# Performance work log

Hardware: AMD Instinct MI355X
Metric: run time of the kernel (lower is better)

The kernel has to match this reference:

```python
import jax, jax.numpy as jnp
import numpy as np

ODIM = 8192      # output dim (slice target)
MSIZE = 64       # tile size
N_BLOCKS = 1024  # size of shared block bank


def setup_inputs() -> dict:
    key = jax.random.key(0)
    k1, k2, k3, k4 = jax.random.split(key, 4)
    x = jax.random.normal(k1, (256, 8192), dtype=jnp.float32)
    # bank of msize x msize module blocks (scaled like fan-in init)
    blocks = jax.random.normal(k2, (N_BLOCKS, MSIZE, MSIZE), dtype=jnp.float32) * 0.02
    bound = 1.0 / np.sqrt(ODIM).astype(np.float32)
    bias = jax.random.uniform(k3, (ODIM,), dtype=jnp.float32, minval=-bound, maxval=bound)
    # parts: [icount, ocount] indices into the block bank
    parts = jax.random.randint(k4, (128, 128), 0, N_BLOCKS)
    return {"x": x, "blocks": blocks, "bias": bias, "parts": parts}


def reference(x, blocks, bias, parts):
    icount, ocount = parts.shape
    m = blocks.shape[-1]
    # build_mosaic: gather blocks per parts and tile into a dense weight matrix
    fc = blocks[parts]                                   # [ic, oc, m, m]
    fc_mat = fc.transpose(0, 2, 1, 3).reshape(icount * m, ocount * m)
    # idim (8192) is divisible by msize, so pad is identity (rem == 0 branch)
    y = x @ fc_mat                                       # [B, oc*m]
    y = y[..., :ODIM] + bias                             # slice + bias; post = Identity
    return y
```

## Files before the change

kernel.cpp:

```cpp
#include <hip/hip_runtime.h>
#include <stdint.h>

#define BATCH 256
#define IDIM  8192
#define ODIM  8192
#define MS    64
#define IC    128
#define OC    128
#define NB    1024

#define TM 128
#define TN 128
#define KSPLIT 4
#define IB_PER (IC / KSPLIT)

typedef __bf16 bf16x8 __attribute__((ext_vector_type(8)));
typedef float  floatx4 __attribute__((ext_vector_type(4)));

__device__ __forceinline__ void async_load16(unsigned short* lds_p, const unsigned short* g_p) {
    __builtin_amdgcn_global_load_lds(
        (const __attribute__((address_space(1))) unsigned int*)g_p,
        (__attribute__((address_space(3))) unsigned int*)lds_p,
        16, 0, 0);
}

__device__ __forceinline__ unsigned short f32_to_bf16(float f) {
    unsigned int u = __float_as_uint(f);
    u += 0x7FFFu + ((u >> 16) & 1u);
    return (unsigned short)(u >> 16);
}

__global__ void k_convert(const float* __restrict__ x, const float* __restrict__ blocks,
                          unsigned short* __restrict__ xb, unsigned short* __restrict__ bt) {
    __shared__ float tile[MS][MS + 1];
    int b = blockIdx.x;
    if (b < NB) {
        const float4* src4 = (const float4*)(blocks + (size_t)b * MS * MS);
        unsigned short* dst = bt + (size_t)b * MS * MS;
        #pragma unroll
        for (int i = 0; i < 4; ++i) {
            int slot = i * 256 + threadIdx.x;
            int r = slot >> 4, c4 = (slot & 15) * 4;
            float4 v = src4[slot];
            tile[r][c4 + 0] = v.x; tile[r][c4 + 1] = v.y;
            tile[r][c4 + 2] = v.z; tile[r][c4 + 3] = v.w;
        }
        __syncthreads();
        #pragma unroll
        for (int i = 0; i < 2; ++i) {
            int slot = i * 256 + threadIdx.x;
            int c = slot >> 3, o = slot & 7;
            union { unsigned short s[8]; uint4 v; } u;
            #pragma unroll
            for (int j = 0; j < 8; ++j) u.s[j] = f32_to_bf16(tile[o * 8 + j][c]);
            *(uint4*)(dst + c * MS + o * 8) = u.v;
        }
    } else {
        int t = (b - NB) * 256 + threadIdx.x;
        const float4* x4 = (const float4*)x;
        float4 a = x4[2 * t], bb = x4[2 * t + 1];
        union { unsigned short s[8]; uint4 v; } u;
        u.s[0] = f32_to_bf16(a.x);  u.s[1] = f32_to_bf16(a.y);
        u.s[2] = f32_to_bf16(a.z);  u.s[3] = f32_to_bf16(a.w);
        u.s[4] = f32_to_bf16(bb.x); u.s[5] = f32_to_bf16(bb.y);
        u.s[6] = f32_to_bf16(bb.z); u.s[7] = f32_to_bf16(bb.w);
        ((uint4*)xb)[t] = u.v;
    }
}

__global__ __launch_bounds__(256, 2)
void k_mosaic_gemm(const unsigned short* __restrict__ xb,
                   const unsigned short* __restrict__ bt,
                   const int* __restrict__ parts,
                   float* __restrict__ partial) {
    __shared__ __align__(16) unsigned short a_lds[TM * MS];
    __shared__ __align__(16) unsigned short b_lds[TN * MS];

    const int tid  = threadIdx.x;
    const int lane = tid & 63;
    const int wave = tid >> 6;
    const int wrow = wave >> 1;
    const int wcol = wave & 1;
    const int nt = blockIdx.x;
    const int mt = blockIdx.y;
    const int ks = blockIdx.z;

    const int m0  = mt * TM;
    const int ob0 = nt * (TN / MS);
    const int ib0 = ks * IB_PER;

    const int row  = lane & 15;
    const int quad = lane >> 4;

    int a_off[2][4], b_off[2][4];
    #pragma unroll
    for (int kk = 0; kk < 2; ++kk) {
        int oct = kk * 4 + quad;
        #pragma unroll
        for (int mi = 0; mi < 4; ++mi) {
            int r = wrow * 64 + mi * 16 + row;
            a_off[kk][mi] = r * MS + ((oct ^ (r & 7)) << 3);
        }
        #pragma unroll
        for (int ni = 0; ni < 4; ++ni) {
            int n = wcol * 64 + ni * 16 + row;
            b_off[kk][ni] = n * MS + ((oct ^ (n & 7)) << 3);
        }
    }

    floatx4 acc[4][4];
    #pragma unroll
    for (int mi = 0; mi < 4; ++mi)
        #pragma unroll
        for (int ni = 0; ni < 4; ++ni)
            acc[mi][ni] = (floatx4){0.f, 0.f, 0.f, 0.f};

    for (int ib = ib0; ib < ib0 + IB_PER; ++ib) {
        int p0 = parts[ib * OC + ob0];
        int p1 = parts[ib * OC + ob0 + 1];

        #pragma unroll
        for (int j = 0; j < 4; ++j) {
            int slot = j * 256 + tid;
            int m = slot >> 3;
            int oct = (slot & 7) ^ (m & 7);
            async_load16(&a_lds[slot * 8],
                         xb + (size_t)(m0 + m) * IDIM + ib * MS + oct * 8);
        }
        #pragma unroll
        for (int j = 0; j < 4; ++j) {
            int slot = j * 256 + tid;
            int n = slot >> 3;
            int oct = (slot & 7) ^ (n & 7);
            int p = (j < 2) ? p0 : p1;
            async_load16(&b_lds[slot * 8],
                         bt + (size_t)p * (MS * MS) + (n & 63) * MS + oct * 8);
        }
        __syncthreads();

        #pragma unroll
        for (int kk = 0; kk < 2; ++kk) {
            bf16x8 af[4], bfr[4];
            #pragma unroll
            for (int mi = 0; mi < 4; ++mi)
                af[mi] = *(const bf16x8*)&a_lds[a_off[kk][mi]];
            #pragma unroll
            for (int ni = 0; ni < 4; ++ni)
                bfr[ni] = *(const bf16x8*)&b_lds[b_off[kk][ni]];
            #pragma unroll
            for (int mi = 0; mi < 4; ++mi)
                #pragma unroll
                for (int ni = 0; ni < 4; ++ni)
                    acc[mi][ni] = __builtin_amdgcn_mfma_f32_16x16x32_bf16(
                        af[mi], bfr[ni], acc[mi][ni], 0, 0, 0);
        }
        __syncthreads();
    }

    float* out = partial + (size_t)ks * BATCH * ODIM;
    #pragma unroll
    for (int mi = 0; mi < 4; ++mi)
        #pragma unroll
        for (int ni = 0; ni < 4; ++ni)
            #pragma unroll
            for (int r = 0; r < 4; ++r) {
                int rowg = m0 + wrow * 64 + mi * 16 + quad * 4 + r;
                int colg = nt * TN + wcol * 64 + ni * 16 + row;
                out[(size_t)rowg * ODIM + colg] = acc[mi][ni][r];
            }
}

__global__ void k_reduce_bias(const float* __restrict__ partial,
                              const float* __restrict__ bias,
                              float* __restrict__ out) {
    int t = blockIdx.x * 256 + threadIdx.x;
    const float4* b4 = (const float4*)bias;
    float4 c = b4[t & (ODIM / 4 - 1)];
    float4 r = {c.x, c.y, c.z, c.w};
    #pragma unroll
    for (int k = 0; k < KSPLIT; ++k) {
        const float4* p = (const float4*)(partial + (size_t)k * BATCH * ODIM);
        float4 a = p[t];
        r.x += a.x; r.y += a.y; r.z += a.z; r.w += a.w;
    }
    ((float4*)out)[t] = r;
}

extern "C" void kernel_launch(void* const* d_in, const int* in_sizes, int n_in,
                              void* d_out, int out_size, void* d_ws, size_t ws_size,
                              hipStream_t stream) {
    const float* x      = (const float*)d_in[0];
    const float* blocks = (const float*)d_in[1];
    const float* bias   = (const float*)d_in[2];
    const int*   parts  = (const int*)d_in[3];
    float* out = (float*)d_out;

    char* ws = (char*)d_ws;
    unsigned short* xb      = (unsigned short*)ws;
    unsigned short* btb     = (unsigned short*)(ws + (4u << 20));
    float*          partial = (float*)(ws + (12u << 20));

    k_convert<<<NB + (BATCH * IDIM) / (256 * 8), 256, 0, stream>>>(x, blocks, xb, btb);
    k_mosaic_gemm<<<dim3(ODIM / TN, BATCH / TM, KSPLIT), 256, 0, stream>>>(xb, btb, parts, partial);
    k_reduce_bias<<<(BATCH * ODIM) / (256 * 4), 256, 0, stream>>>(partial, bias, out);
}
```

Measured before the change: 125.5 us.

## Replace split-K partial buffer and reduce kernel with atomic accumulation into output

Removes the separate reduce+bias kernel and the partial-sum workspace. The output is initialised with bias inside the convert kernel, and the GEMM accumulates split-K results into it with float atomicAdd. The M tile grows to the full batch (256) and KSPLIT doubles to 8, which keeps the block count the same and lets each block reuse its B tile across all rows. The cost is atomic traffic, nondeterministic summation order, and roughly double the accumulator registers per thread, which may reduce occupancy.

```diff
diff --git a/kernel.cpp b/kernel.cpp
--- a/kernel.cpp
+++ b/kernel.cpp
@@ -9,9 +9,9 @@
 #define OC    128
 #define NB    1024
 
-#define TM 128
+#define TM 256
 #define TN 128
-#define KSPLIT 4
+#define KSPLIT 8
 #define IB_PER (IC / KSPLIT)
 
 typedef __bf16 bf16x8 __attribute__((ext_vector_type(8)));
@@ -30,8 +30,11 @@
     return (unsigned short)(u >> 16);
 }
 
+#define XCONV_BLKS ((BATCH * IDIM) / (256 * 8))
 __global__ void k_convert(const float* __restrict__ x, const float* __restrict__ blocks,
-                          unsigned short* __restrict__ xb, unsigned short* __restrict__ bt) {
+                          const float* __restrict__ bias,
+                          unsigned short* __restrict__ xb, unsigned short* __restrict__ bt,
+                          float* __restrict__ out) {
     __shared__ float tile[MS][MS + 1];
     int b = blockIdx.x;
     if (b < NB) {
@@ -55,7 +58,7 @@
             for (int j = 0; j < 8; ++j) u.s[j] = f32_to_bf16(tile[o * 8 + j][c]);
             *(uint4*)(dst + c * MS + o * 8) = u.v;
         }
-    } else {
+    } else if (b < NB + XCONV_BLKS) {
         int t = (b - NB) * 256 + threadIdx.x;
         const float4* x4 = (const float4*)x;
         float4 a = x4[2 * t], bb = x4[2 * t + 1];
@@ -65,6 +68,15 @@
         u.s[4] = f32_to_bf16(bb.x); u.s[5] = f32_to_bf16(bb.y);
         u.s[6] = f32_to_bf16(bb.z); u.s[7] = f32_to_bf16(bb.w);
         ((uint4*)xb)[t] = u.v;
+    } else {
+        int r = b - NB - XCONV_BLKS;
+        const float4* b4 = (const float4*)bias;
+        float4* o4 = (float4*)out + (size_t)r * (ODIM / 4);
+        #pragma unroll
+        for (int j = 0; j < 8; ++j) {
+            int c = j * 256 + threadIdx.x;
+            o4[c] = b4[c];
+        }
     }
 }
 
@@ -72,7 +84,7 @@
 void k_mosaic_gemm(const unsigned short* __restrict__ xb,
                    const unsigned short* __restrict__ bt,
                    const int* __restrict__ parts,
-                   float* __restrict__ partial) {
+                   float* __restrict__ out) {
     __shared__ __align__(16) unsigned short a_lds[TM * MS];
     __shared__ __align__(16) unsigned short b_lds[TN * MS];
 
@@ -82,23 +94,21 @@
     const int wrow = wave >> 1;
     const int wcol = wave & 1;
     const int nt = blockIdx.x;
-    const int mt = blockIdx.y;
-    const int ks = blockIdx.z;
+    const int ks = blockIdx.y;
 
-    const int m0  = mt * TM;
     const int ob0 = nt * (TN / MS);
     const int ib0 = ks * IB_PER;
 
     const int row  = lane & 15;
     const int quad = lane >> 4;
 
-    int a_off[2][4], b_off[2][4];
+    int a_off[2][8], b_off[2][4];
     #pragma unroll
     for (int kk = 0; kk < 2; ++kk) {
         int oct = kk * 4 + quad;
         #pragma unroll
-        for (int mi = 0; mi < 4; ++mi) {
-            int r = wrow * 64 + mi * 16 + row;
+        for (int mi = 0; mi < 8; ++mi) {
+            int r = wrow * 128 + mi * 16 + row;
             a_off[kk][mi] = r * MS + ((oct ^ (r & 7)) << 3);
         }
         #pragma unroll
@@ -108,9 +118,9 @@
         }
     }
 
-    floatx4 acc[4][4];
+    floatx4 acc[8][4];
     #pragma unroll
-    for (int mi = 0; mi < 4; ++mi)
+    for (int mi = 0; mi < 8; ++mi)
         #pragma unroll
         for (int ni = 0; ni < 4; ++ni)
             acc[mi][ni] = (floatx4){0.f, 0.f, 0.f, 0.f};
@@ -120,12 +130,12 @@
         int p1 = parts[ib * OC + ob0 + 1];
 
         #pragma unroll
-        for (int j = 0; j < 4; ++j) {
+        for (int j = 0; j < 8; ++j) {
             int slot = j * 256 + tid;
             int m = slot >> 3;
             int oct = (slot & 7) ^ (m & 7);
             async_load16(&a_lds[slot * 8],
-                         xb + (size_t)(m0 + m) * IDIM + ib * MS + oct * 8);
+                         xb + (size_t)m * IDIM + ib * MS + oct * 8);
         }
         #pragma unroll
         for (int j = 0; j < 4; ++j) {
@@ -140,15 +150,15 @@
 
         #pragma unroll
         for (int kk = 0; kk < 2; ++kk) {
-            bf16x8 af[4], bfr[4];
+            bf16x8 af[8], bfr[4];
             #pragma unroll
-            for (int mi = 0; mi < 4; ++mi)
+            for (int mi = 0; mi < 8; ++mi)
                 af[mi] = *(const bf16x8*)&a_lds[a_off[kk][mi]];
             #pragma unroll
             for (int ni = 0; ni < 4; ++ni)
                 bfr[ni] = *(const bf16x8*)&b_lds[b_off[kk][ni]];
             #pragma unroll
-            for (int mi = 0; mi < 4; ++mi)
+            for (int mi = 0; mi < 8; ++mi)
                 #pragma unroll
                 for (int ni = 0; ni < 4; ++ni)
                     acc[mi][ni] = __builtin_amdgcn_mfma_f32_16x16x32_bf16(
@@ -157,33 +167,16 @@
         __syncthreads();
     }
 
-    float* out = partial + (size_t)ks * BATCH * ODIM;
     #pragma unroll
-    for (int mi = 0; mi < 4; ++mi)
+    for (int mi = 0; mi < 8; ++mi)
         #pragma unroll
         for (int ni = 0; ni < 4; ++ni)
             #pragma unroll
             for (int r = 0; r < 4; ++r) {
-                int rowg = m0 + wrow * 64 + mi * 16 + quad * 4 + r;
+                int rowg = wrow * 128 + mi * 16 + quad * 4 + r;
                 int colg = nt * TN + wcol * 64 + ni * 16 + row;
-                out[(size_t)rowg * ODIM + colg] = acc[mi][ni][r];
+                atomicAdd(&out[(size_t)rowg * ODIM + colg], acc[mi][ni][r]);
             }
-}
-
-__global__ void k_reduce_bias(const float* __restrict__ partial,
-                              const float* __restrict__ bias,
-                              float* __restrict__ out) {
-    int t = blockIdx.x * 256 + threadIdx.x;
-    const float4* b4 = (const float4*)bias;
-    float4 c = b4[t & (ODIM / 4 - 1)];
-    float4 r = {c.x, c.y, c.z, c.w};
-    #pragma unroll
-    for (int k = 0; k < KSPLIT; ++k) {
-        const float4* p = (const float4*)(partial + (size_t)k * BATCH * ODIM);
-        float4 a = p[t];
-        r.x += a.x; r.y += a.y; r.z += a.z; r.w += a.w;
-    }
-    ((float4*)out)[t] = r;
 }
 
 extern "C" void kernel_launch(void* const* d_in, const int* in_sizes, int n_in,
@@ -196,11 +189,9 @@
     float* out = (float*)d_out;
 
     char* ws = (char*)d_ws;
-    unsigned short* xb      = (unsigned short*)ws;
-    unsigned short* btb     = (unsigned short*)(ws + (4u << 20));
-    float*          partial = (float*)(ws + (12u << 20));
+    unsigned short* xb  = (unsigned short*)ws;
+    unsigned short* btb = (unsigned short*)(ws + (4u << 20));
 
-    k_convert<<<NB + (BATCH * IDIM) / (256 * 8), 256, 0, stream>>>(x, blocks, xb, btb);
-    k_mosaic_gemm<<<dim3(ODIM / TN, BATCH / TM, KSPLIT), 256, 0, stream>>>(xb, btb, parts, partial);
-    k_reduce_bias<<<(BATCH * ODIM) / (256 * 4), 256, 0, stream>>>(partial, bias, out);
+    k_convert<<<NB + XCONV_BLKS + BATCH, 256, 0, stream>>>(x, blocks, bias, xb, btb, out);
+    k_mosaic_gemm<<<dim3(ODIM / TN, KSPLIT), 256, 0, stream>>>(xb, btb, parts, out);
 }
```

Result: slower. 153.7 us (+22.5%).

## Pre-swizzle operands into MFMA fragment layout and load directly to registers

Applied to the files above, without the earlier changes.

The convert kernel now writes x and the block bank in MFMA fragment order and transposes the parts table, so the GEMM can drop LDS staging and barriers and load bf16x8 fragments straight from global memory into registers. The GEMM becomes a per-64-column tile over all 256 rows (4 waves, each 64 rows), with register double-buffering of the next two K blocks. This removes the LDS round trip and syncthreads, but A is no longer shared through LDS across waves. Each workgroup reads the full A slice from global/L2, and the grid shrinks to 512 workgroups.

```diff
diff --git a/kernel.cpp b/kernel.cpp
--- a/kernel.cpp
+++ b/kernel.cpp
@@ -9,20 +9,11 @@
 #define OC    128
 #define NB    1024
 
-#define TM 128
-#define TN 128
 #define KSPLIT 4
-#define IB_PER (IC / KSPLIT)
+#define NIB (IC / KSPLIT)
 
 typedef __bf16 bf16x8 __attribute__((ext_vector_type(8)));
 typedef float  floatx4 __attribute__((ext_vector_type(4)));
-
-__device__ __forceinline__ void async_load16(unsigned short* lds_p, const unsigned short* g_p) {
-    __builtin_amdgcn_global_load_lds(
-        (const __attribute__((address_space(1))) unsigned int*)g_p,
-        (__attribute__((address_space(3))) unsigned int*)lds_p,
-        16, 0, 0);
-}
 
 __device__ __forceinline__ unsigned short f32_to_bf16(float f) {
     unsigned int u = __float_as_uint(f);
@@ -30,13 +21,16 @@
     return (unsigned short)(u >> 16);
 }
 
+#define XCONV_BLKS 1024
+#define PT_BLKS 64
 __global__ void k_convert(const float* __restrict__ x, const float* __restrict__ blocks,
-                          unsigned short* __restrict__ xb, unsigned short* __restrict__ bt) {
+                          const int* __restrict__ parts,
+                          unsigned short* __restrict__ xa, unsigned short* __restrict__ bbuf,
+                          int* __restrict__ pT) {
     __shared__ float tile[MS][MS + 1];
     int b = blockIdx.x;
     if (b < NB) {
         const float4* src4 = (const float4*)(blocks + (size_t)b * MS * MS);
-        unsigned short* dst = bt + (size_t)b * MS * MS;
         #pragma unroll
         for (int i = 0; i < 4; ++i) {
             int slot = i * 256 + threadIdx.x;
@@ -46,67 +40,63 @@
             tile[r][c4 + 2] = v.z; tile[r][c4 + 3] = v.w;
         }
         __syncthreads();
+        unsigned short* dst = bbuf + (size_t)b * 4096;
         #pragma unroll
         for (int i = 0; i < 2; ++i) {
-            int slot = i * 256 + threadIdx.x;
-            int c = slot >> 3, o = slot & 7;
+            int oo = i * 256 + threadIdx.x;
+            int L = oo & 63, kk = (oo >> 6) & 1, ng = (oo >> 7) & 3;
+            int row = L & 15, quad = L >> 4;
             union { unsigned short s[8]; uint4 v; } u;
             #pragma unroll
-            for (int j = 0; j < 8; ++j) u.s[j] = f32_to_bf16(tile[o * 8 + j][c]);
-            *(uint4*)(dst + c * MS + o * 8) = u.v;
+            for (int j = 0; j < 8; ++j)
+                u.s[j] = f32_to_bf16(tile[kk * 32 + quad * 8 + j][ng * 16 + row]);
+            *(uint4*)(dst + oo * 8) = u.v;
         }
+    } else if (b < NB + XCONV_BLKS) {
+        int o = (b - NB) * 256 + threadIdx.x;
+        int L = o & 63, kk = (o >> 6) & 1, ib = (o >> 7) & 127, g = o >> 14;
+        int m  = g * 16 + (L & 15);
+        int k0 = ib * 64 + kk * 32 + (L >> 4) * 8;
+        const float* src = x + (size_t)m * IDIM + k0;
+        float4 a = *(const float4*)src, c = *(const float4*)(src + 4);
+        union { unsigned short s[8]; uint4 v; } u;
+        u.s[0] = f32_to_bf16(a.x); u.s[1] = f32_to_bf16(a.y);
+        u.s[2] = f32_to_bf16(a.z); u.s[3] = f32_to_bf16(a.w);
+        u.s[4] = f32_to_bf16(c.x); u.s[5] = f32_to_bf16(c.y);
+        u.s[6] = f32_to_bf16(c.z); u.s[7] = f32_to_bf16(c.w);
+        *(uint4*)(xa + (size_t)o * 8) = u.v;
     } else {
-        int t = (b - NB) * 256 + threadIdx.x;
-        const float4* x4 = (const float4*)x;
-        float4 a = x4[2 * t], bb = x4[2 * t + 1];
-        union { unsigned short s[8]; uint4 v; } u;
-        u.s[0] = f32_to_bf16(a.x);  u.s[1] = f32_to_bf16(a.y);
-        u.s[2] = f32_to_bf16(a.z);  u.s[3] = f32_to_bf16(a.w);
-        u.s[4] = f32_to_bf16(bb.x); u.s[5] = f32_to_bf16(bb.y);
-        u.s[6] = f32_to_bf16(bb.z); u.s[7] = f32_to_bf16(bb.w);
-        ((uint4*)xb)[t] = u.v;
+        int t = (b - NB - XCONV_BLKS) * 256 + threadIdx.x;
+        int oc = t >> 7, ic = t & 127;
+        pT[t] = parts[ic * OC + oc];
     }
 }
 
 __global__ __launch_bounds__(256, 2)
-void k_mosaic_gemm(const unsigned short* __restrict__ xb,
-                   const unsigned short* __restrict__ bt,
-                   const int* __restrict__ parts,
+void k_mosaic_gemm(const unsigned short* __restrict__ xa,
+                   const unsigned short* __restrict__ bbuf,
+                   const int* __restrict__ pT,
                    float* __restrict__ partial) {
-    __shared__ __align__(16) unsigned short a_lds[TM * MS];
-    __shared__ __align__(16) unsigned short b_lds[TN * MS];
-
     const int tid  = threadIdx.x;
     const int lane = tid & 63;
-    const int wave = tid >> 6;
-    const int wrow = wave >> 1;
-    const int wcol = wave & 1;
-    const int nt = blockIdx.x;
-    const int mt = blockIdx.y;
-    const int ks = blockIdx.z;
-
-    const int m0  = mt * TM;
-    const int ob0 = nt * (TN / MS);
-    const int ib0 = ks * IB_PER;
+    const int w    = tid >> 6;
+    const int ob   = blockIdx.x;
+    const int ks   = blockIdx.y;
+    const int ib0  = ks * NIB;
 
     const int row  = lane & 15;
     const int quad = lane >> 4;
 
-    int a_off[2][4], b_off[2][4];
+    const unsigned short* abase[4][2];
     #pragma unroll
-    for (int kk = 0; kk < 2; ++kk) {
-        int oct = kk * 4 + quad;
+    for (int mi = 0; mi < 4; ++mi)
         #pragma unroll
-        for (int mi = 0; mi < 4; ++mi) {
-            int r = wrow * 64 + mi * 16 + row;
-            a_off[kk][mi] = r * MS + ((oct ^ (r & 7)) << 3);
-        }
-        #pragma unroll
-        for (int ni = 0; ni < 4; ++ni) {
-            int n = wcol * 64 + ni * 16 + row;
-            b_off[kk][ni] = n * MS + ((oct ^ (n & 7)) << 3);
-        }
-    }
+        for (int kk = 0; kk < 2; ++kk)
+            abase[mi][kk] = xa + (size_t)(w * 4 + mi) * 131072 + kk * 512 + lane * 8;
+
+    const int* pp = pT + ob * 128 + ib0;
+
+    bf16x8 ac[4][2], bc[4][2], an[4][2], bn[4][2];
 
     floatx4 acc[4][4];
     #pragma unroll
@@ -115,46 +105,33 @@
         for (int ni = 0; ni < 4; ++ni)
             acc[mi][ni] = (floatx4){0.f, 0.f, 0.f, 0.f};
 
-    for (int ib = ib0; ib < ib0 + IB_PER; ++ib) {
-        int p0 = parts[ib * OC + ob0];
-        int p1 = parts[ib * OC + ob0 + 1];
+#define LOAD_A(dst, ib_) do { \
+    _Pragma("unroll") for (int mi = 0; mi < 4; ++mi) \
+    _Pragma("unroll") for (int kk = 0; kk < 2; ++kk) \
+        dst[mi][kk] = *(const bf16x8*)(abase[mi][kk] + (size_t)(ib0 + (ib_)) * 1024); } while (0)
+#define LOAD_B(dst, p_) do { \
+    const unsigned short* bp = bbuf + (size_t)(p_) * 4096 + lane * 8; \
+    _Pragma("unroll") for (int ng = 0; ng < 4; ++ng) \
+    _Pragma("unroll") for (int kk = 0; kk < 2; ++kk) \
+        dst[ng][kk] = *(const bf16x8*)(bp + (ng * 2 + kk) * 512); } while (0)
+#define DO_MFMA(a_, b_) do { \
+    _Pragma("unroll") for (int kk = 0; kk < 2; ++kk) \
+    _Pragma("unroll") for (int mi = 0; mi < 4; ++mi) \
+    _Pragma("unroll") for (int ni = 0; ni < 4; ++ni) \
+        acc[mi][ni] = __builtin_amdgcn_mfma_f32_16x16x32_bf16(a_[mi][kk], b_[ni][kk], acc[mi][ni], 0, 0, 0); } while (0)
 
-        #pragma unroll
-        for (int j = 0; j < 4; ++j) {
-            int slot = j * 256 + tid;
-            int m = slot >> 3;
-            int oct = (slot & 7) ^ (m & 7);
-            async_load16(&a_lds[slot * 8],
-                         xb + (size_t)(m0 + m) * IDIM + ib * MS + oct * 8);
-        }
-        #pragma unroll
-        for (int j = 0; j < 4; ++j) {
-            int slot = j * 256 + tid;
-            int n = slot >> 3;
-            int oct = (slot & 7) ^ (n & 7);
-            int p = (j < 2) ? p0 : p1;
-            async_load16(&b_lds[slot * 8],
-                         bt + (size_t)p * (MS * MS) + (n & 63) * MS + oct * 8);
-        }
-        __syncthreads();
+    LOAD_A(ac, 0);
+    LOAD_B(bc, pp[0]);
 
-        #pragma unroll
-        for (int kk = 0; kk < 2; ++kk) {
-            bf16x8 af[4], bfr[4];
-            #pragma unroll
-            for (int mi = 0; mi < 4; ++mi)
-                af[mi] = *(const bf16x8*)&a_lds[a_off[kk][mi]];
-            #pragma unroll
-            for (int ni = 0; ni < 4; ++ni)
-                bfr[ni] = *(const bf16x8*)&b_lds[b_off[kk][ni]];
-            #pragma unroll
-            for (int mi = 0; mi < 4; ++mi)
-                #pragma unroll
-                for (int ni = 0; ni < 4; ++ni)
-                    acc[mi][ni] = __builtin_amdgcn_mfma_f32_16x16x32_bf16(
-                        af[mi], bfr[ni], acc[mi][ni], 0, 0, 0);
-        }
-        __syncthreads();
+    for (int ii = 0; ii < NIB; ii += 2) {
+        int i1 = (ii + 1 < NIB) ? ii + 1 : NIB - 1;
+        int i2 = (ii + 2 < NIB) ? ii + 2 : NIB - 1;
+        LOAD_A(an, i1);
+        LOAD_B(bn, pp[i1]);
+        DO_MFMA(ac, bc);
+        LOAD_A(ac, i2);
+        LOAD_B(bc, pp[i2]);
+        DO_MFMA(an, bn);
     }
 
     float* out = partial + (size_t)ks * BATCH * ODIM;
@@ -164,8 +141,8 @@
         for (int ni = 0; ni < 4; ++ni)
             #pragma unroll
             for (int r = 0; r < 4; ++r) {
-                int rowg = m0 + wrow * 64 + mi * 16 + quad * 4 + r;
-                int colg = nt * TN + wcol * 64 + ni * 16 + row;
+                int rowg = w * 64 + mi * 16 + quad * 4 + r;
+                int colg = ob * 64 + ni * 16 + row;
                 out[(size_t)rowg * ODIM + colg] = acc[mi][ni][r];
             }
 }
@@ -196,11 +173,12 @@
     float* out = (float*)d_out;
 
     char* ws = (char*)d_ws;
-    unsigned short* xb      = (unsigned short*)ws;
-    unsigned short* btb     = (unsigned short*)(ws + (4u << 20));
-    float*          partial = (float*)(ws + (12u << 20));
+    unsigned short* xa      = (unsigned short*)ws;
+    unsigned short* bbuf    = (unsigned short*)(ws + (4u << 20));
+    int*            pTr     = (int*)(ws + (12u << 20));
+    float*          partial = (float*)(ws + (13u << 20));
 
-    k_convert<<<NB + (BATCH * IDIM) / (256 * 8), 256, 0, stream>>>(x, blocks, xb, btb);
-    k_mosaic_gemm<<<dim3(ODIM / TN, BATCH / TM, KSPLIT), 256, 0, stream>>>(xb, btb, parts, partial);
+    k_convert<<<NB + XCONV_BLKS + PT_BLKS, 256, 0, stream>>>(x, blocks, parts, xa, bbuf, pTr);
+    k_mosaic_gemm<<<dim3(OC, KSPLIT), 256, 0, stream>>>(xa, bbuf, pTr, partial);
     k_reduce_bias<<<(BATCH * ODIM) / (256 * 4), 256, 0, stream>>>(partial, bias, out);
 }
```

Result: slower. 153.2 us (+22.1%).

## Double-buffer LDS tiles and prefetch transposed parts indices via shuffles

Applied to the files above, without the earlier changes.

Converts the GEMM main loop to a two-stage LDS double buffer: the next K-block's async global-to-LDS loads are issued before computing the current one, using a partial vmcnt wait instead of a full sync. The parts index table is transposed in the convert kernel so each wave loads all its block indices up front and broadcasts them with shuffles, removing per-iteration scalar index loads. This doubles LDS use per workgroup, which may limit occupancy under the 2-block launch bound.

```diff
diff --git a/kernel.cpp b/kernel.cpp
--- a/kernel.cpp
+++ b/kernel.cpp
@@ -12,10 +12,12 @@
 #define TM 128
 #define TN 128
 #define KSPLIT 4
-#define IB_PER (IC / KSPLIT)
+#define NIB (IC / KSPLIT)
 
 typedef __bf16 bf16x8 __attribute__((ext_vector_type(8)));
 typedef float  floatx4 __attribute__((ext_vector_type(4)));
+
+#define WAITCNT_VM(n) ((((n) & 15) | (((n) >> 4) << 14)) | 0x70 | 0xF00)
 
 __device__ __forceinline__ void async_load16(unsigned short* lds_p, const unsigned short* g_p) {
     __builtin_amdgcn_global_load_lds(
@@ -30,8 +32,12 @@
     return (unsigned short)(u >> 16);
 }
 
+#define XCONV_BLKS 1024
+#define PT_BLKS 64
 __global__ void k_convert(const float* __restrict__ x, const float* __restrict__ blocks,
-                          unsigned short* __restrict__ xb, unsigned short* __restrict__ bt) {
+                          const int* __restrict__ parts,
+                          unsigned short* __restrict__ xb, unsigned short* __restrict__ bt,
+                          int* __restrict__ pT) {
     __shared__ float tile[MS][MS + 1];
     int b = blockIdx.x;
     if (b < NB) {
@@ -55,7 +61,7 @@
             for (int j = 0; j < 8; ++j) u.s[j] = f32_to_bf16(tile[o * 8 + j][c]);
             *(uint4*)(dst + c * MS + o * 8) = u.v;
         }
-    } else {
+    } else if (b < NB + XCONV_BLKS) {
         int t = (b - NB) * 256 + threadIdx.x;
         const float4* x4 = (const float4*)x;
         float4 a = x4[2 * t], bb = x4[2 * t + 1];
@@ -65,16 +71,20 @@
         u.s[4] = f32_to_bf16(bb.x); u.s[5] = f32_to_bf16(bb.y);
         u.s[6] = f32_to_bf16(bb.z); u.s[7] = f32_to_bf16(bb.w);
         ((uint4*)xb)[t] = u.v;
+    } else {
+        int t = (b - NB - XCONV_BLKS) * 256 + threadIdx.x;
+        int oc = t >> 7, ic = t & 127;
+        pT[t] = parts[ic * OC + oc];
     }
 }
 
 __global__ __launch_bounds__(256, 2)
 void k_mosaic_gemm(const unsigned short* __restrict__ xb,
                    const unsigned short* __restrict__ bt,
-                   const int* __restrict__ parts,
+                   const int* __restrict__ pT,
                    float* __restrict__ partial) {
-    __shared__ __align__(16) unsigned short a_lds[TM * MS];
-    __shared__ __align__(16) unsigned short b_lds[TN * MS];
+    __shared__ __align__(16) unsigned short a_lds[2][TM * MS];
+    __shared__ __align__(16) unsigned short b_lds[2][TN * MS];
 
     const int tid  = threadIdx.x;
     const int lane = tid & 63;
@@ -86,11 +96,18 @@
     const int ks = blockIdx.z;
 
     const int m0  = mt * TM;
-    const int ob0 = nt * (TN / MS);
-    const int ib0 = ks * IB_PER;
+    const int ob0 = nt * 2;
+    const int ib0 = ks * NIB;
 
     const int row  = lane & 15;
     const int quad = lane >> 4;
+
+    int pv0 = 0, pv1 = 0;
+    {
+        int li = lane & 31;
+        pv0 = pT[ob0 * IC + ib0 + li];
+        pv1 = pT[(ob0 + 1) * IC + ib0 + li];
+    }
 
     int a_off[2][4], b_off[2][4];
     #pragma unroll
@@ -115,47 +132,59 @@
         for (int ni = 0; ni < 4; ++ni)
             acc[mi][ni] = (floatx4){0.f, 0.f, 0.f, 0.f};
 
-    for (int ib = ib0; ib < ib0 + IB_PER; ++ib) {
-        int p0 = parts[ib * OC + ob0];
-        int p1 = parts[ib * OC + ob0 + 1];
-
-        #pragma unroll
-        for (int j = 0; j < 4; ++j) {
-            int slot = j * 256 + tid;
-            int m = slot >> 3;
-            int oct = (slot & 7) ^ (m & 7);
-            async_load16(&a_lds[slot * 8],
-                         xb + (size_t)(m0 + m) * IDIM + ib * MS + oct * 8);
-        }
-        #pragma unroll
-        for (int j = 0; j < 4; ++j) {
-            int slot = j * 256 + tid;
-            int n = slot >> 3;
-            int oct = (slot & 7) ^ (n & 7);
-            int p = (j < 2) ? p0 : p1;
-            async_load16(&b_lds[slot * 8],
-                         bt + (size_t)p * (MS * MS) + (n & 63) * MS + oct * 8);
-        }
-        __syncthreads();
-
-        #pragma unroll
-        for (int kk = 0; kk < 2; ++kk) {
-            bf16x8 af[4], bfr[4];
-            #pragma unroll
-            for (int mi = 0; mi < 4; ++mi)
-                af[mi] = *(const bf16x8*)&a_lds[a_off[kk][mi]];
-            #pragma unroll
-            for (int ni = 0; ni < 4; ++ni)
-                bfr[ni] = *(const bf16x8*)&b_lds[b_off[kk][ni]];
-            #pragma unroll
-            for (int mi = 0; mi < 4; ++mi)
-                #pragma unroll
-                for (int ni = 0; ni < 4; ++ni)
-                    acc[mi][ni] = __builtin_amdgcn_mfma_f32_16x16x32_bf16(
-                        af[mi], bfr[ni], acc[mi][ni], 0, 0, 0);
-        }
-        __syncthreads();
-    }
+#define STAGE(buf, ib_, p0_, p1_) do {                                        \
+    _Pragma("unroll")                                                         \
+    for (int j = 0; j < 4; ++j) {                                             \
+        int slot = j * 256 + tid;                                             \
+        int m = slot >> 3;                                                    \
+        int oct = (slot & 7) ^ (m & 7);                                       \
+        async_load16(&a_lds[buf][slot * 8],                                   \
+                     xb + (size_t)(m0 + m) * IDIM + (ib_) * MS + oct * 8);    \
+    }                                                                         \
+    _Pragma("unroll")                                                         \
+    for (int j = 0; j < 4; ++j) {                                             \
+        int slot = j * 256 + tid;                                             \
+        int n = slot >> 3;                                                    \
+        int oct = (slot & 7) ^ (n & 7);                                       \
+        int p = (j < 2) ? (p0_) : (p1_);                                      \
+        async_load16(&b_lds[buf][slot * 8],                                   \
+                     bt + (size_t)p * (MS * MS) + (n & 63) * MS + oct * 8);   \
+    } } while (0)
+
+#define COMPUTE(buf) do {                                                     \
+    _Pragma("unroll")                                                         \
+    for (int kk = 0; kk < 2; ++kk) {                                          \
+        bf16x8 af[4], bfr[4];                                                 \
+        _Pragma("unroll")                                                     \
+        for (int mi = 0; mi < 4; ++mi)                                        \
+            af[mi] = *(const bf16x8*)&a_lds[buf][a_off[kk][mi]];              \
+        _Pragma("unroll")                                                     \
+        for (int ni = 0; ni < 4; ++ni)                                        \
+            bfr[ni] = *(const bf16x8*)&b_lds[buf][b_off[kk][ni]];             \
+        _Pragma("unroll")                                                     \
+        for (int mi = 0; mi < 4; ++mi)                                        \
+            _Pragma("unroll")                                                 \
+            for (int ni = 0; ni < 4; ++ni)                                    \
+                acc[mi][ni] = __builtin_amdgcn_mfma_f32_16x16x32_bf16(        \
+                    af[mi], bfr[ni], acc[mi][ni], 0, 0, 0);                   \
+    } } while (0)
+
+    {
+        int p0 = __shfl(pv0, 0), p1 = __shfl(pv1, 0);
+        STAGE(0, ib0 + 0, p0, p1);
+    }
+
+    for (int i = 0; i < NIB - 1; ++i) {
+        int p0n = __shfl(pv0, i + 1), p1n = __shfl(pv1, i + 1);
+        STAGE((i + 1) & 1, ib0 + i + 1, p0n, p1n);
+        __builtin_amdgcn_s_waitcnt(WAITCNT_VM(8));
+        __builtin_amdgcn_s_barrier();
+        COMPUTE(i & 1);
+        __builtin_amdgcn_s_barrier();
+    }
+    __builtin_amdgcn_s_waitcnt(WAITCNT_VM(0));
+    __builtin_amdgcn_s_barrier();
+    COMPUTE((NIB - 1) & 1);
 
     float* out = partial + (size_t)ks * BATCH * ODIM;
     #pragma unroll
@@ -198,9 +227,10 @@
     char* ws = (char*)d_ws;
     unsigned short* xb      = (unsigned short*)ws;
     unsigned short* btb     = (unsigned short*)(ws + (4u << 20));
-    float*          partial = (float*)(ws + (12u << 20));
-
-    k_convert<<<NB + (BATCH * IDIM) / (256 * 8), 256, 0, stream>>>(x, blocks, xb, btb);
-    k_mosaic_gemm<<<dim3(ODIM / TN, BATCH / TM, KSPLIT), 256, 0, stream>>>(xb, btb, parts, partial);
+    int*            pTr     = (int*)(ws + (12u << 20));
+    float*          partial = (float*)(ws + (13u << 20));
+
+    k_convert<<<NB + XCONV_BLKS + PT_BLKS, 256, 0, stream>>>(x, blocks, parts, xb, btb, pTr);
+    k_mosaic_gemm<<<dim3(ODIM / TN, BATCH / TM, KSPLIT), 256, 0, stream>>>(xb, btb, pTr, partial);
     k_reduce_bias<<<(BATCH * ODIM) / (256 * 4), 256, 0, stream>>>(partial, bias, out);
 }
```

New measurement: 120.6 us. 1.04x faster.
